# Kernel tuning notes

Measured on AMD Instinct MI355X. Metric: run time of the kernel, lower is better.

Reference implementation:

```python
import jax, jax.numpy as jnp
import numpy as np

B, V, E, W = 1024, 50257, 128, 4  # batch, vocab, embed, CBOW window

def setup_inputs() -> dict:
    key = jax.random.key(0)
    k1, k2, k3, k4 = jax.random.split(key, 4)
    # near-one-hot averaged bag-of-words: 2*W context indices per row, each weighted 1/(2*W)
    ctx_idx = jax.random.randint(k1, (B, 2 * W), 0, V)
    xs = jnp.zeros((B, V), dtype=jnp.float32).at[jnp.arange(B)[:, None], ctx_idx].add(1.0 / (2 * W))
    metric = jax.random.normal(k2, (E, E), dtype=jnp.float32)  # unused by forward, kept for signature fidelity
    EMBEDM = jax.random.normal(k3, (V, E), dtype=jnp.float32)
    embed2vocab = jax.random.normal(k4, (E, V), dtype=jnp.float32)
    return {"xs": xs, "metric": metric, "EMBEDM": EMBEDM, "embed2vocab": embed2vocab}

def reference(xs, metric, EMBEDM, embed2vocab):
    # [B,V] @ [V,E] -> [B,E]  (gather+average in disguise: xs is sparse n-hot)
    xsembeds = xs @ EMBEDM
    # [B,E] @ [E,V] -> [B,V], then row-wise log_softmax
    xsouts = xsembeds @ embed2vocab
    return jax.nn.log_softmax(xsouts, axis=1)
```

## Files before the change

### kernel.cpp

```cpp
#include <hip/hip_runtime.h>
#include <hip/hip_bf16.h>

#define B_ROWS 1024
#define V_DIM 50257
#define E_DIM 128
#define V_PAD 50304
#define NCT 786

typedef __attribute__((ext_vector_type(8))) short short8;
typedef __attribute__((ext_vector_type(4))) float float4v;

__global__ void k0_transpose(const float* __restrict__ e2v,
                             __hip_bfloat16* __restrict__ e2vT) {
    __shared__ float t[32][33];
    const int v0 = blockIdx.x * 32;
    const int k0 = blockIdx.y * 32;
    const int c = threadIdx.x & 31;
    const int r = threadIdx.x >> 5;
#pragma unroll
    for (int i = 0; i < 4; ++i) {
        const int k = k0 + r + i * 8;
        const int v = v0 + c;
        t[r + i * 8][c] = (v < V_DIM) ? e2v[(size_t)k * V_DIM + v] : 0.0f;
    }
    __syncthreads();
#pragma unroll
    for (int i = 0; i < 4; ++i) {
        const int rv = r + i * 8;
        e2vT[(size_t)(v0 + rv) * E_DIM + k0 + c] = __float2bfloat16(t[c][rv]);
    }
}

__global__ void k1_embed(const float* __restrict__ xs,
                         const float* __restrict__ EM,
                         __hip_bfloat16* __restrict__ xse) {
    const int b = blockIdx.x;
    const int tid = threadIdx.x;
    __shared__ int nzv[64];
    __shared__ float nzval[64];
    __shared__ int nzcount;
    if (tid == 0) nzcount = 0;
    __syncthreads();

    const size_t base = (size_t)b * V_DIM;
    auto note = [&](int v, float val) {
        if (val != 0.0f) {
            int s = atomicAdd(&nzcount, 1);
            if (s < 64) { nzv[s] = v; nzval[s] = val; }
        }
    };

    const int h = (int)((4 - (base & 3)) & 3);
    if (tid < h) note(tid, xs[base + tid]);
    const int n4 = (V_DIM - h) >> 2;
    const float4* xv = reinterpret_cast<const float4*>(xs + base + h);
    for (int j = tid; j < n4; j += 256) {
        float4 x = xv[j];
        if (x.x != 0.0f || x.y != 0.0f || x.z != 0.0f || x.w != 0.0f) {
            const int v = h + 4 * j;
            note(v + 0, x.x);
            note(v + 1, x.y);
            note(v + 2, x.z);
            note(v + 3, x.w);
        }
    }
    for (int i = h + n4 * 4 + tid; i < V_DIM; i += 256) note(i, xs[base + i]);
    __syncthreads();

    int cnt = nzcount;
    if (cnt > 64) cnt = 64;
    if (tid < E_DIM) {
        float a = 0.0f;
        for (int s = 0; s < cnt; ++s)
            a += nzval[s] * EM[(size_t)nzv[s] * E_DIM + tid];
        xse[(size_t)b * E_DIM + tid] = __float2bfloat16(a);
    }
}

#define GEMM_TILE_BODY(xse, e2vT)                                              \
    __shared__ unsigned short As[128][136];                                    \
    __shared__ unsigned short Bs[64][136];                                     \
    const int tid = threadIdx.x;                                               \
    const int m0 = blockIdx.x * 128;                                           \
    const int v0 = blockIdx.y * 64;                                            \
    const unsigned short* gA = reinterpret_cast<const unsigned short*>(xse);   \
    const unsigned short* gB = reinterpret_cast<const unsigned short*>(e2vT);  \
    _Pragma("unroll")                                                          \
    for (int i = 0; i < 8; ++i) {                                              \
        const int c = tid + i * 256;                                           \
        const int row = c >> 4;                                                \
        const int kc = (c & 15) << 3;                                          \
        *reinterpret_cast<int4*>(&As[row][kc]) =                               \
            *reinterpret_cast<const int4*>(gA + (size_t)(m0 + row) * E_DIM + kc); \
    }                                                                          \
    _Pragma("unroll")                                                          \
    for (int i = 0; i < 4; ++i) {                                              \
        const int c = tid + i * 256;                                           \
        const int row = c >> 4;                                                \
        const int kc = (c & 15) << 3;                                          \
        *reinterpret_cast<int4*>(&Bs[row][kc]) =                               \
            *reinterpret_cast<const int4*>(gB + (size_t)(v0 + row) * E_DIM + kc); \
    }                                                                          \
    __syncthreads();                                                           \
    const int w = tid >> 6;                                                    \
    const int lane = tid & 63;                                                 \
    const int q = lane >> 4;                                                   \
    const int l16 = lane & 15;                                                 \
    const int wm = w * 32;                                                     \
    float4v acc[2][4];                                                         \
    _Pragma("unroll")                                                          \
    for (int mi = 0; mi < 2; ++mi)                                             \
        _Pragma("unroll")                                                      \
        for (int ni = 0; ni < 4; ++ni)                                         \
            acc[mi][ni] = (float4v){0.0f, 0.0f, 0.0f, 0.0f};                   \
    _Pragma("unroll")                                                          \
    for (int kk = 0; kk < 128; kk += 32) {                                     \
        const int ko = kk + q * 8;                                             \
        short8 a0 = *reinterpret_cast<const short8*>(&As[wm + l16][ko]);       \
        short8 a1 = *reinterpret_cast<const short8*>(&As[wm + 16 + l16][ko]);  \
        _Pragma("unroll")                                                      \
        for (int ni = 0; ni < 4; ++ni) {                                       \
            short8 bf = *reinterpret_cast<const short8*>(&Bs[ni * 16 + l16][ko]); \
            acc[0][ni] = __builtin_amdgcn_mfma_f32_16x16x32_bf16(a0, bf, acc[0][ni], 0, 0, 0); \
            acc[1][ni] = __builtin_amdgcn_mfma_f32_16x16x32_bf16(a1, bf, acc[1][ni], 0, 0, 0); \
        }                                                                      \
    }

__global__ __launch_bounds__(256) void kb_pass1(
        const __hip_bfloat16* __restrict__ xse,
        const __hip_bfloat16* __restrict__ e2vT,
        float* __restrict__ pmax,
        float* __restrict__ psum) {
    GEMM_TILE_BODY(xse, e2vT)

#pragma unroll
    for (int mi = 0; mi < 2; ++mi) {
#pragma unroll
        for (int r = 0; r < 4; ++r) {
            float mx = -INFINITY;
#pragma unroll
            for (int ni = 0; ni < 4; ++ni) {
                const int col = v0 + ni * 16 + l16;
                const float x = (col < V_DIM) ? acc[mi][ni][r] : -INFINITY;
                mx = fmaxf(mx, x);
            }
            mx = fmaxf(mx, __shfl_xor(mx, 1));
            mx = fmaxf(mx, __shfl_xor(mx, 2));
            mx = fmaxf(mx, __shfl_xor(mx, 4));
            mx = fmaxf(mx, __shfl_xor(mx, 8));
            float s = 0.0f;
#pragma unroll
            for (int ni = 0; ni < 4; ++ni) {
                const int col = v0 + ni * 16 + l16;
                const float x = (col < V_DIM) ? acc[mi][ni][r] : -INFINITY;
                s += __expf(x - mx);
            }
            s += __shfl_xor(s, 1);
            s += __shfl_xor(s, 2);
            s += __shfl_xor(s, 4);
            s += __shfl_xor(s, 8);
            if (l16 == 0) {
                const int row = m0 + wm + mi * 16 + q * 4 + r;
                pmax[(size_t)row * NCT + blockIdx.y] = mx;
                psum[(size_t)row * NCT + blockIdx.y] = s;
            }
        }
    }
}

__global__ void kc_combine(const float* __restrict__ pmax,
                           const float* __restrict__ psum,
                           float* __restrict__ stats) {
    const int b = blockIdx.x;
    const int tid = threadIdx.x;
    float m = -INFINITY, s = 0.0f;
    for (int j = tid; j < NCT; j += 256) {
        const float mj = pmax[(size_t)b * NCT + j];
        const float sj = psum[(size_t)b * NCT + j];
        if (mj > m) { s = s * __expf(m - mj) + sj; m = mj; }
        else        { s += sj * __expf(mj - m); }
    }
    __shared__ float rm[256], rs[256];
    rm[tid] = m; rs[tid] = s;
    __syncthreads();
    for (int off = 128; off > 0; off >>= 1) {
        if (tid < off) {
            const float m2 = rm[tid + off], s2 = rs[tid + off];
            const float M = fmaxf(m, m2);
            s = s * __expf(m - M) + s2 * __expf(m2 - M);
            m = M;
            rm[tid] = m; rs[tid] = s;
        }
        __syncthreads();
    }
    if (tid == 0) stats[b] = m + __logf(s);
}

__global__ __launch_bounds__(256) void kd_pass2(
        const __hip_bfloat16* __restrict__ xse,
        const __hip_bfloat16* __restrict__ e2vT,
        const float* __restrict__ stats,
        float* __restrict__ out) {
    GEMM_TILE_BODY(xse, e2vT)

#pragma unroll
    for (int mi = 0; mi < 2; ++mi) {
        const int rbase = m0 + wm + mi * 16 + q * 4;
        float l[4];
#pragma unroll
        for (int r = 0; r < 4; ++r) l[r] = stats[rbase + r];
#pragma unroll
        for (int ni = 0; ni < 4; ++ni) {
            const int col = v0 + ni * 16 + l16;
            if (col < V_DIM) {
#pragma unroll
                for (int r = 0; r < 4; ++r)
                    out[(size_t)(rbase + r) * V_DIM + col] = acc[mi][ni][r] - l[r];
            }
        }
    }
}

extern "C" void kernel_launch(void* const* d_in, const int* in_sizes, int n_in,
                              void* d_out, int out_size, void* d_ws, size_t ws_size,
                              hipStream_t stream) {
    const float* xs  = (const float*)d_in[0];
    const float* EM  = (const float*)d_in[2];
    const float* e2v = (const float*)d_in[3];
    float* out = (float*)d_out;

    char* ws = (char*)d_ws;
    __hip_bfloat16* e2vT = (__hip_bfloat16*)ws;
    size_t off = (size_t)V_PAD * E_DIM * 2;
    __hip_bfloat16* xse = (__hip_bfloat16*)(ws + off);
    off += (size_t)B_ROWS * E_DIM * 2;
    float* pmax = (float*)(ws + off);
    off += (size_t)B_ROWS * NCT * 4;
    float* psum = (float*)(ws + off);
    off += (size_t)B_ROWS * NCT * 4;
    float* stats = (float*)(ws + off);

    hipLaunchKernelGGL(k0_transpose, dim3(V_PAD / 32, E_DIM / 32), dim3(256), 0, stream, e2v, e2vT);
    hipLaunchKernelGGL(k1_embed, dim3(B_ROWS), dim3(256), 0, stream, xs, EM, xse);
    hipLaunchKernelGGL(kb_pass1, dim3(B_ROWS / 128, NCT), dim3(256), 0, stream, xse, e2vT, pmax, psum);
    hipLaunchKernelGGL(kc_combine, dim3(B_ROWS), dim3(256), 0, stream, pmax, psum, stats);
    hipLaunchKernelGGL(kd_pass2, dim3(B_ROWS / 128, NCT), dim3(256), 0, stream, xse, e2vT, stats, out);
}
```

Before: 458.4 us.

## Make GEMM blocks loop over vocab tiles with register-held A and double-buffered B

Each GEMM block now walks 8 consecutive 64-column vocab tiles instead of one. The A fragments stay in registers and the next B tile is prefetched into a double-buffered shared array. Pass 1 keeps an online max/sum per row across tiles, which cuts the partial-stat array by 8x, and the combine kernel becomes a single-wave shuffle reduction. This removes per-tile A reloads and launch overhead, but the grid is much smaller (8x99 blocks), which may underfill the GPU.

```diff
diff --git a/kernel.cpp b/kernel.cpp
--- a/kernel.cpp
+++ b/kernel.cpp
@@ -6,6 +6,10 @@
 #define E_DIM 128
 #define V_PAD 50304
 #define NCT 786
+#define TPC 8
+#define NCH ((NCT + TPC - 1) / TPC)
+
+static_assert(NCH * TPC >= NCT, "chunking must cover all tiles");
 
 typedef __attribute__((ext_vector_type(8))) short short8;
 typedef __attribute__((ext_vector_type(4))) float float4v;
@@ -77,94 +81,177 @@
     }
 }
 
-#define GEMM_TILE_BODY(xse, e2vT)                                              \
-    __shared__ unsigned short As[128][136];                                    \
-    __shared__ unsigned short Bs[64][136];                                     \
-    const int tid = threadIdx.x;                                               \
-    const int m0 = blockIdx.x * 128;                                           \
-    const int v0 = blockIdx.y * 64;                                            \
-    const unsigned short* gA = reinterpret_cast<const unsigned short*>(xse);   \
-    const unsigned short* gB = reinterpret_cast<const unsigned short*>(e2vT);  \
-    _Pragma("unroll")                                                          \
-    for (int i = 0; i < 8; ++i) {                                              \
-        const int c = tid + i * 256;                                           \
-        const int row = c >> 4;                                                \
-        const int kc = (c & 15) << 3;                                          \
-        *reinterpret_cast<int4*>(&As[row][kc]) =                               \
-            *reinterpret_cast<const int4*>(gA + (size_t)(m0 + row) * E_DIM + kc); \
-    }                                                                          \
-    _Pragma("unroll")                                                          \
-    for (int i = 0; i < 4; ++i) {                                              \
-        const int c = tid + i * 256;                                           \
-        const int row = c >> 4;                                                \
-        const int kc = (c & 15) << 3;                                          \
-        *reinterpret_cast<int4*>(&Bs[row][kc]) =                               \
-            *reinterpret_cast<const int4*>(gB + (size_t)(v0 + row) * E_DIM + kc); \
-    }                                                                          \
-    __syncthreads();                                                           \
-    const int w = tid >> 6;                                                    \
-    const int lane = tid & 63;                                                 \
-    const int q = lane >> 4;                                                   \
-    const int l16 = lane & 15;                                                 \
-    const int wm = w * 32;                                                     \
-    float4v acc[2][4];                                                         \
-    _Pragma("unroll")                                                          \
-    for (int mi = 0; mi < 2; ++mi)                                             \
-        _Pragma("unroll")                                                      \
-        for (int ni = 0; ni < 4; ++ni)                                         \
-            acc[mi][ni] = (float4v){0.0f, 0.0f, 0.0f, 0.0f};                   \
-    _Pragma("unroll")                                                          \
-    for (int kk = 0; kk < 128; kk += 32) {                                     \
-        const int ko = kk + q * 8;                                             \
-        short8 a0 = *reinterpret_cast<const short8*>(&As[wm + l16][ko]);       \
-        short8 a1 = *reinterpret_cast<const short8*>(&As[wm + 16 + l16][ko]);  \
-        _Pragma("unroll")                                                      \
-        for (int ni = 0; ni < 4; ++ni) {                                       \
-            short8 bf = *reinterpret_cast<const short8*>(&Bs[ni * 16 + l16][ko]); \
-            acc[0][ni] = __builtin_amdgcn_mfma_f32_16x16x32_bf16(a0, bf, acc[0][ni], 0, 0, 0); \
-            acc[1][ni] = __builtin_amdgcn_mfma_f32_16x16x32_bf16(a1, bf, acc[1][ni], 0, 0, 0); \
-        }                                                                      \
-    }
-
-__global__ __launch_bounds__(256) void kb_pass1(
+template <bool PASS2>
+__global__ __launch_bounds__(256, 3) void gemm_pass(
         const __hip_bfloat16* __restrict__ xse,
         const __hip_bfloat16* __restrict__ e2vT,
         float* __restrict__ pmax,
-        float* __restrict__ psum) {
-    GEMM_TILE_BODY(xse, e2vT)
-
-#pragma unroll
-    for (int mi = 0; mi < 2; ++mi) {
-#pragma unroll
-        for (int r = 0; r < 4; ++r) {
-            float mx = -INFINITY;
+        float* __restrict__ psum,
+        const float* __restrict__ stats,
+        float* __restrict__ out) {
+    __shared__ __align__(16) unsigned short Bs[2][64][136];
+    const int tid = threadIdx.x;
+    const int m0 = blockIdx.x * 128;
+    const int ch = blockIdx.y;
+    const int t0 = ch * TPC;
+    const int tend = (t0 + TPC < NCT) ? (t0 + TPC) : NCT;
+
+    const int w = tid >> 6;
+    const int lane = tid & 63;
+    const int q = lane >> 4;
+    const int l16 = lane & 15;
+    const int wm = w * 32;
+
+    const unsigned short* gA = reinterpret_cast<const unsigned short*>(xse);
+    const unsigned short* gB = reinterpret_cast<const unsigned short*>(e2vT);
+
+    short8 af[2][4];
+#pragma unroll
+    for (int mi = 0; mi < 2; ++mi)
+#pragma unroll
+        for (int kt = 0; kt < 4; ++kt)
+            af[mi][kt] = *reinterpret_cast<const short8*>(
+                gA + (size_t)(m0 + wm + mi * 16 + l16) * E_DIM + kt * 32 + q * 8);
+
+    float lse[2][4];
+    if constexpr (PASS2) {
+#pragma unroll
+        for (int mi = 0; mi < 2; ++mi)
+#pragma unroll
+            for (int r = 0; r < 4; ++r)
+                lse[mi][r] = stats[m0 + wm + mi * 16 + q * 4 + r];
+    }
+
+    float mrun[2][4], srun[2][4];
+    if constexpr (!PASS2) {
+#pragma unroll
+        for (int mi = 0; mi < 2; ++mi)
+#pragma unroll
+            for (int r = 0; r < 4; ++r) {
+                mrun[mi][r] = -INFINITY;
+                srun[mi][r] = 0.0f;
+            }
+    }
+
+    int4 g[4];
+    {
+        const int v0 = t0 * 64;
+#pragma unroll
+        for (int i = 0; i < 4; ++i) {
+            const int p = tid + i * 256;
+            const int row = p >> 4;
+            const int kc = (p & 15) << 3;
+            g[i] = *reinterpret_cast<const int4*>(gB + (size_t)(v0 + row) * E_DIM + kc);
+        }
+    }
+
+    for (int t = t0; t < tend; ++t) {
+        const int buf = (t - t0) & 1;
+        const int v0 = t * 64;
+
+#pragma unroll
+        for (int i = 0; i < 4; ++i) {
+            const int p = tid + i * 256;
+            const int row = p >> 4;
+            const int kc = (p & 15) << 3;
+            *reinterpret_cast<int4*>(&Bs[buf][row][kc]) = g[i];
+        }
+        if (t + 1 < tend) {
+            const int v1 = (t + 1) * 64;
+#pragma unroll
+            for (int i = 0; i < 4; ++i) {
+                const int p = tid + i * 256;
+                const int row = p >> 4;
+                const int kc = (p & 15) << 3;
+                g[i] = *reinterpret_cast<const int4*>(gB + (size_t)(v1 + row) * E_DIM + kc);
+            }
+        }
+        __syncthreads();
+
+        float4v acc[2][4];
+#pragma unroll
+        for (int mi = 0; mi < 2; ++mi)
+#pragma unroll
+            for (int ni = 0; ni < 4; ++ni)
+                acc[mi][ni] = (float4v){0.0f, 0.0f, 0.0f, 0.0f};
+
+#pragma unroll
+        for (int kt = 0; kt < 4; ++kt) {
+            const int ko = kt * 32 + q * 8;
 #pragma unroll
             for (int ni = 0; ni < 4; ++ni) {
-                const int col = v0 + ni * 16 + l16;
-                const float x = (col < V_DIM) ? acc[mi][ni][r] : -INFINITY;
-                mx = fmaxf(mx, x);
-            }
-            mx = fmaxf(mx, __shfl_xor(mx, 1));
-            mx = fmaxf(mx, __shfl_xor(mx, 2));
-            mx = fmaxf(mx, __shfl_xor(mx, 4));
-            mx = fmaxf(mx, __shfl_xor(mx, 8));
-            float s = 0.0f;
-#pragma unroll
-            for (int ni = 0; ni < 4; ++ni) {
-                const int col = v0 + ni * 16 + l16;
-                const float x = (col < V_DIM) ? acc[mi][ni][r] : -INFINITY;
-                s += __expf(x - mx);
-            }
-            s += __shfl_xor(s, 1);
-            s += __shfl_xor(s, 2);
-            s += __shfl_xor(s, 4);
-            s += __shfl_xor(s, 8);
-            if (l16 == 0) {
-                const int row = m0 + wm + mi * 16 + q * 4 + r;
-                pmax[(size_t)row * NCT + blockIdx.y] = mx;
-                psum[(size_t)row * NCT + blockIdx.y] = s;
-            }
-        }
+                short8 bf = *reinterpret_cast<const short8*>(&Bs[buf][ni * 16 + l16][ko]);
+                acc[0][ni] = __builtin_amdgcn_mfma_f32_16x16x32_bf16(af[0][kt], bf, acc[0][ni], 0, 0, 0);
+                acc[1][ni] = __builtin_amdgcn_mfma_f32_16x16x32_bf16(af[1][kt], bf, acc[1][ni], 0, 0, 0);
+            }
+        }
+
+        if constexpr (!PASS2) {
+            const bool full = (v0 + 64 <= V_DIM);
+#pragma unroll
+            for (int mi = 0; mi < 2; ++mi)
+#pragma unroll
+                for (int r = 0; r < 4; ++r) {
+                    float x0 = acc[mi][0][r];
+                    float x1 = acc[mi][1][r];
+                    float x2 = acc[mi][2][r];
+                    float x3 = acc[mi][3][r];
+                    if (!full) {
+                        x0 = (v0 + 0 * 16 + l16 < V_DIM) ? x0 : -INFINITY;
+                        x1 = (v0 + 1 * 16 + l16 < V_DIM) ? x1 : -INFINITY;
+                        x2 = (v0 + 2 * 16 + l16 < V_DIM) ? x2 : -INFINITY;
+                        x3 = (v0 + 3 * 16 + l16 < V_DIM) ? x3 : -INFINITY;
+                    }
+                    const float pm = fmaxf(fmaxf(x0, x1), fmaxf(x2, x3));
+                    const float M = fmaxf(mrun[mi][r], pm);
+                    if (M == -INFINITY) {
+                        srun[mi][r] = 0.0f;
+                    } else {
+                        const float sadd = __expf(x0 - M) + __expf(x1 - M) +
+                                           __expf(x2 - M) + __expf(x3 - M);
+                        srun[mi][r] = srun[mi][r] * __expf(mrun[mi][r] - M) + sadd;
+                        mrun[mi][r] = M;
+                    }
+                }
+        } else {
+#pragma unroll
+            for (int mi = 0; mi < 2; ++mi) {
+                const int rbase = m0 + wm + mi * 16 + q * 4;
+#pragma unroll
+                for (int ni = 0; ni < 4; ++ni) {
+                    const int col = v0 + ni * 16 + l16;
+                    if (col < V_DIM) {
+#pragma unroll
+                        for (int r = 0; r < 4; ++r)
+                            out[(size_t)(rbase + r) * V_DIM + col] = acc[mi][ni][r] - lse[mi][r];
+                    }
+                }
+            }
+        }
+    }
+
+    if constexpr (!PASS2) {
+#pragma unroll
+        for (int mi = 0; mi < 2; ++mi)
+#pragma unroll
+            for (int r = 0; r < 4; ++r) {
+                float mv = mrun[mi][r];
+                float sv = srun[mi][r];
+#pragma unroll
+                for (int d = 1; d < 16; d <<= 1) {
+                    const float m2 = __shfl_xor(mv, d);
+                    const float s2 = __shfl_xor(sv, d);
+                    const float M = fmaxf(mv, m2);
+                    sv = (M == -INFINITY) ? 0.0f
+                                          : sv * __expf(mv - M) + s2 * __expf(m2 - M);
+                    mv = M;
+                }
+                if (l16 == 0) {
+                    const int row = m0 + wm + mi * 16 + q * 4 + r;
+                    pmax[(size_t)row * NCH + ch] = mv;
+                    psum[(size_t)row * NCH + ch] = sv;
+                }
+            }
     }
 }
 
@@ -172,53 +259,24 @@
                            const float* __restrict__ psum,
                            float* __restrict__ stats) {
     const int b = blockIdx.x;
-    const int tid = threadIdx.x;
+    const int lane = threadIdx.x;
     float m = -INFINITY, s = 0.0f;
-    for (int j = tid; j < NCT; j += 256) {
-        const float mj = pmax[(size_t)b * NCT + j];
-        const float sj = psum[(size_t)b * NCT + j];
-        if (mj > m) { s = s * __expf(m - mj) + sj; m = mj; }
-        else        { s += sj * __expf(mj - m); }
-    }
-    __shared__ float rm[256], rs[256];
-    rm[tid] = m; rs[tid] = s;
-    __syncthreads();
-    for (int off = 128; off > 0; off >>= 1) {
-        if (tid < off) {
-            const float m2 = rm[tid + off], s2 = rs[tid + off];
-            const float M = fmaxf(m, m2);
-            s = s * __expf(m - M) + s2 * __expf(m2 - M);
-            m = M;
-            rm[tid] = m; rs[tid] = s;
-        }
-        __syncthreads();
-    }
-    if (tid == 0) stats[b] = m + __logf(s);
-}
-
-__global__ __launch_bounds__(256) void kd_pass2(
-        const __hip_bfloat16* __restrict__ xse,
-        const __hip_bfloat16* __restrict__ e2vT,
-        const float* __restrict__ stats,
-        float* __restrict__ out) {
-    GEMM_TILE_BODY(xse, e2vT)
-
-#pragma unroll
-    for (int mi = 0; mi < 2; ++mi) {
-        const int rbase = m0 + wm + mi * 16 + q * 4;
-        float l[4];
-#pragma unroll
-        for (int r = 0; r < 4; ++r) l[r] = stats[rbase + r];
-#pragma unroll
-        for (int ni = 0; ni < 4; ++ni) {
-            const int col = v0 + ni * 16 + l16;
-            if (col < V_DIM) {
-#pragma unroll
-                for (int r = 0; r < 4; ++r)
-                    out[(size_t)(rbase + r) * V_DIM + col] = acc[mi][ni][r] - l[r];
-            }
-        }
-    }
+    for (int j = lane; j < NCH; j += 64) {
+        const float mj = pmax[(size_t)b * NCH + j];
+        const float sj = psum[(size_t)b * NCH + j];
+        const float M = fmaxf(m, mj);
+        s = (M == -INFINITY) ? 0.0f : s * __expf(m - M) + sj * __expf(mj - M);
+        m = M;
+    }
+#pragma unroll
+    for (int d = 1; d < 64; d <<= 1) {
+        const float m2 = __shfl_xor(m, d);
+        const float s2 = __shfl_xor(s, d);
+        const float M = fmaxf(m, m2);
+        s = (M == -INFINITY) ? 0.0f : s * __expf(m - M) + s2 * __expf(m2 - M);
+        m = M;
+    }
+    if (lane == 0) stats[b] = m + __logf(s);
 }
 
 extern "C" void kernel_launch(void* const* d_in, const int* in_sizes, int n_in,
@@ -235,14 +293,16 @@
     __hip_bfloat16* xse = (__hip_bfloat16*)(ws + off);
     off += (size_t)B_ROWS * E_DIM * 2;
     float* pmax = (float*)(ws + off);
-    off += (size_t)B_ROWS * NCT * 4;
+    off += (size_t)B_ROWS * NCH * 4;
     float* psum = (float*)(ws + off);
-    off += (size_t)B_ROWS * NCT * 4;
+    off += (size_t)B_ROWS * NCH * 4;
     float* stats = (float*)(ws + off);
 
-    hipLaunchKernelGGL(k0_transpose, dim3(V_PAD / 32, E_DIM / 32), dim3(256), 0, stream, e2v, e2vT);
-    hipLaunchKernelGGL(k1_embed, dim3(B_ROWS), dim3(256), 0, stream, xs, EM, xse);
-    hipLaunchKernelGGL(kb_pass1, dim3(B_ROWS / 128, NCT), dim3(256), 0, stream, xse, e2vT, pmax, psum);
-    hipLaunchKernelGGL(kc_combine, dim3(B_ROWS), dim3(256), 0, stream, pmax, psum, stats);
-    hipLaunchKernelGGL(kd_pass2, dim3(B_ROWS / 128, NCT), dim3(256), 0, stream, xse, e2vT, stats, out);
-}
+    k0_transpose<<<dim3(V_PAD / 32, E_DIM / 32), dim3(256), 0, stream>>>(e2v, e2vT);
+    k1_embed<<<dim3(B_ROWS), dim3(256), 0, stream>>>(xs, EM, xse);
+    gemm_pass<false><<<dim3(B_ROWS / 128, NCH), dim3(256), 0, stream>>>(
+        xse, e2vT, pmax, psum, nullptr, nullptr);
+    kc_combine<<<dim3(B_ROWS), dim3(64), 0, stream>>>(pmax, psum, stats);
+    gemm_pass<true><<<dim3(B_ROWS / 128, NCH), dim3(256), 0, stream>>>(
+        xse, e2vT, nullptr, nullptr, stats, out);
+}
```

Result: slower. 518.7 us (+13.2%).
